# Kernel optimization log

Hardware: AMD Instinct MI355X
Metric: run time of the kernel (lower is better)

Reference implementation:

```python
import jax, jax.numpy as jnp
import numpy as np


def _prelu(x, a):
    return jnp.where(x >= 0, x, a * x)


def _conv1x1(x, w, b, a):
    # x: [N,C,H,W], w: [O,C], b: [O] -> PReLU(conv1x1(x))
    y = jnp.einsum('oc,nchw->nohw', w, x) + b[None, :, None, None]
    return _prelu(y, a)


def setup_inputs() -> dict:
    key = jax.random.key(0)
    ks = jax.random.split(key, 8)
    N, C, H, W = 4, 128, 64, 64
    Cr = C // 2  # reduction=2
    sC = 1.0 / np.sqrt(C)
    x = jax.random.normal(ks[0], (N, C, H, W), dtype=jnp.float32)
    w1 = jax.random.normal(ks[1], (Cr, C), dtype=jnp.float32) * sC
    b1 = jnp.zeros((Cr,), dtype=jnp.float32)
    a1 = jnp.asarray(0.25, dtype=jnp.float32)  # PReLU (single shared slope)
    w2 = jax.random.normal(ks[2], (Cr, C), dtype=jnp.float32) * sC
    b2 = jnp.zeros((Cr,), dtype=jnp.float32)
    a2 = jnp.asarray(0.25, dtype=jnp.float32)
    wa = jax.random.normal(ks[3], (C, C), dtype=jnp.float32) * sC
    ba = jnp.zeros((C,), dtype=jnp.float32)
    aa = jnp.asarray(0.25, dtype=jnp.float32)
    return {"x": x, "w1": w1, "b1": b1, "a1": a1,
            "w2": w2, "b2": b2, "a2": a2,
            "wa": wa, "ba": ba, "aa": aa}


def reference(x, w1, b1, a1, w2, b2, a2, wa, ba, aa):
    N, C, H, W = x.shape
    HW = H * W
    e1 = _conv1x1(x, w1, b1, a1).reshape(N, -1, HW)   # [N,Cr,HW]
    e2 = _conv1x1(x, w2, b2, a2).reshape(N, -1, HW)   # [N,Cr,HW]
    asm = _conv1x1(x, wa, ba, aa).reshape(N, C, HW)   # [N,C,HW]
    # ksize=1: per-channel outer products summed over channels == single contraction
    score = jnp.einsum('nci,ncj->nij', e1, e2)        # [N,HW,HW]
    score = jax.nn.softmax(score, axis=2)
    out = jnp.einsum('nij,ncj->nci', score, asm)      # [N,C,HW]
    return out.reshape(N, C, H, W)
```

## Files before the change

kernel.cpp:

```cpp
#include <hip/hip_runtime.h>
#include <hip/hip_bf16.h>
#include <stdint.h>


typedef float   f32x16 __attribute__((ext_vector_type(16)));
typedef __bf16  bf16x8 __attribute__((ext_vector_type(8)));
typedef __bf16  bf16x2 __attribute__((ext_vector_type(2)));
typedef unsigned int u32x4 __attribute__((ext_vector_type(4)));
typedef unsigned int u32x2 __attribute__((ext_vector_type(2)));

#define L2E 1.4426950408889634f

#define Q_OFF   (0u)
#define KF_OFF  (2u << 20)
#define VF_OFF  (4u << 20)
#define DEN_OFF (8u << 20)
#define WH_OFF  ((8u << 20) + (1u << 19))
#define WL_OFF  (WH_OFF + (1u << 16))
#define OP_OFF  (9u << 20)

__device__ inline unsigned short f2bf(float f) {
  unsigned u = __builtin_bit_cast(unsigned, f);
  return (unsigned short)((u + 0x7FFFu + ((u >> 16) & 1u)) >> 16);
}
__device__ inline float bf2f(unsigned short h) {
  unsigned u = ((unsigned)h) << 16;
  return __builtin_bit_cast(float, u);
}
__device__ inline unsigned pack2(float a, float b) {
  bf16x2 t = { (__bf16)a, (__bf16)b };
  return __builtin_bit_cast(unsigned, t);
}

__device__ inline void gld_lds16(const void* g, void* l) {
  __builtin_amdgcn_global_load_lds(
      (const __attribute__((address_space(1))) unsigned*)g,
      (__attribute__((address_space(3))) unsigned*)l, 16, 0, 0);
}

__global__ void wcast_kernel(const float* __restrict__ w1, const float* __restrict__ w2,
                             const float* __restrict__ wa, char* __restrict__ ws) {
  int idx = blockIdx.x * 256 + threadIdx.x;
  unsigned short* WH = (unsigned short*)(ws + WH_OFF);
  unsigned short* WL = (unsigned short*)(ws + WL_OFF);
#pragma unroll
  for (int r = 0; r < 4; ++r) {
    int i = r * 8192 + idx;
    int oc = i >> 7, c = i & 127;
    float v = oc < 64 ? w1[oc * 128 + c]
            : (oc < 128 ? w2[(oc - 64) * 128 + c] : wa[(oc - 128) * 128 + c]);
    unsigned short h = f2bf(v);
    WH[i] = h;
    WL[i] = f2bf(v - bf2f(h));
  }
}

__global__ __launch_bounds__(256) void conv_kernel(
    const float* __restrict__ x, char* __restrict__ ws,
    const float* __restrict__ b1, const float* __restrict__ a1,
    const float* __restrict__ b2, const float* __restrict__ a2,
    const float* __restrict__ ba, const float* __restrict__ aa) {
  int bid = blockIdx.x;
  int n = bid >> 7, st = bid & 127;
  int sb = st * 32;
  int tid = threadIdx.x;
  int wid = tid >> 6, lane = tid & 63, l31 = lane & 31, hi = lane >> 5;

  __shared__ float xl[128][36];
  __shared__ float tl[2][64][33];
  float* vl = (float*)xl;

  const float* xb = x + (size_t)n * 128 * 4096;
#pragma unroll
  for (int it = 0; it < 4; ++it) {
    int flat4 = tid + 256 * it;
    int c = flat4 >> 3, s4 = flat4 & 7;
    float4 v = *(const float4*)(xb + (size_t)c * 4096 + sb + s4 * 4);
    *(float4*)&xl[c][s4 * 4] = v;
  }
  __syncthreads();

  const char* WH = ws + WH_OFF;
  const char* WL = ws + WL_OFF;
  int oc0 = wid * 64;

  f32x16 acc[2];
  acc[0] = 0.f; acc[1] = 0.f;
#pragma unroll
  for (int c0 = 0; c0 < 8; ++c0) {
    __bf16 eh[8], el[8];
#pragma unroll
    for (int j = 0; j < 8; ++j) {
      float v = xl[c0 * 16 + hi * 8 + j][l31];
      __bf16 h = (__bf16)v;
      eh[j] = h;
      el[j] = (__bf16)(v - (float)h);
    }
    bf16x8 xh = {eh[0], eh[1], eh[2], eh[3], eh[4], eh[5], eh[6], eh[7]};
    bf16x8 xlo = {el[0], el[1], el[2], el[3], el[4], el[5], el[6], el[7]};
#pragma unroll
    for (int mb = 0; mb < 2; ++mb) {
      size_t wo = (size_t)(oc0 + mb * 32 + l31) * 256 + c0 * 32 + hi * 16;
      bf16x8 wh = *(const bf16x8*)(WH + wo);
      bf16x8 wl = *(const bf16x8*)(WL + wo);
      acc[mb] = __builtin_amdgcn_mfma_f32_32x32x16_bf16(wh, xh, acc[mb], 0, 0, 0);
      acc[mb] = __builtin_amdgcn_mfma_f32_32x32x16_bf16(wh, xlo, acc[mb], 0, 0, 0);
      acc[mb] = __builtin_amdgcn_mfma_f32_32x32x16_bf16(wl, xh, acc[mb], 0, 0, 0);
    }
  }
  __syncthreads();

  if (wid < 2) {
    const float* bb = wid ? b2 : b1;
    float slope = wid ? a2[0] : a1[0];
    float scl = wid ? 1.0f : L2E;
#pragma unroll
    for (int mb = 0; mb < 2; ++mb)
#pragma unroll
      for (int reg = 0; reg < 16; ++reg) {
        int row = mb * 32 + (reg & 3) + 8 * (reg >> 2) + 4 * hi;
        float y = acc[mb][reg] + bb[row];
        y = fmaxf(y, 0.f) + slope * fminf(y, 0.f);
        tl[wid][row][l31] = y * scl;
      }
  } else {
    float slope = aa[0];
#pragma unroll
    for (int mb = 0; mb < 2; ++mb)
#pragma unroll
      for (int reg = 0; reg < 16; ++reg) {
        int dv = (wid - 2) * 64 + mb * 32 + (reg & 3) + 8 * (reg >> 2) + 4 * hi;
        float y = acc[mb][reg] + ba[dv];
        y = fmaxf(y, 0.f) + slope * fminf(y, 0.f);
        vl[dv * 33 + l31] = y;
      }
  }
  __syncthreads();

  if (wid == 0) {
    char* Qg = ws + Q_OFF + (size_t)n * (4096 * 128);
#pragma unroll
    for (int it = 0; it < 4; ++it) {
      int sl = (lane >> 3) + it * 8;
      u32x4 pv;
#pragma unroll
      for (int p = 0; p < 4; ++p)
        pv[p] = pack2(tl[0][(lane & 7) * 8 + 2 * p][sl],
                      tl[0][(lane & 7) * 8 + 2 * p + 1][sl]);
      *(u32x4*)(Qg + (size_t)(sb + sl) * 128 + (lane & 7) * 16) = pv;
    }
  } else if (wid == 1) {
    char* KFb = ws + KF_OFF + (size_t)n * (512 << 10);
    int d0 = (lane & 7) >> 1, hs = lane & 1;
#pragma unroll
    for (int it = 0; it < 4; ++it) {
      int sl = (lane >> 3) + it * 8;
      u32x4 pv;
#pragma unroll
      for (int p = 0; p < 4; ++p)
        pv[p] = pack2(tl[1][(lane & 7) * 8 + 2 * p][sl],
                      tl[1][(lane & 7) * 8 + 2 * p + 1][sl]);
      *(u32x4*)(KFb + ((size_t)(st * 4 + d0) * 64 + hs * 32 + sl) * 16) = pv;
    }
  }
  {
    char* VFb = ws + VF_OFF + (size_t)n * (1u << 20);
#pragma unroll
    for (int r = 0; r < 2; ++r) {
      int u = tid + r * 256;
      int dv = u >> 2, sc = u & 3;
      u32x4 pv;
#pragma unroll
      for (int p = 0; p < 4; ++p)
        pv[p] = pack2(vl[dv * 33 + sc * 8 + 2 * p], vl[dv * 33 + sc * 8 + 2 * p + 1]);
      int unit = st * 8 + (dv >> 5) * 2 + (sc >> 1);
      *(u32x4*)(VFb + ((size_t)unit * 64 + (sc & 1) * 32 + (dv & 31)) * 16) = pv;
    }
  }
}

__global__ __launch_bounds__(256, 3) void attn_kernel(char* __restrict__ ws) {
  int bid = blockIdx.x;
  int split = bid & 7;
  int qt = (bid >> 3) & 31;
  int batch = bid >> 8;
  int tid = threadIdx.x;
  int wid = tid >> 6, lane = tid & 63, l31 = lane & 31, hi = lane >> 5;

  const char* Qb  = ws + Q_OFF  + (size_t)batch * (4096 * 128);
  const char* Kt0 = ws + KF_OFF + (size_t)batch * (512 << 10) +
                    (size_t)(split * 16) * 4096;
  const char* Vt0 = ws + VF_OFF + (size_t)batch * (1u << 20) +
                    (size_t)(split * 16) * 8192;

  __shared__ char sbuf[3][12288];

  int q0 = qt * 128 + wid * 32;
  int lo16 = lane * 16;

  bf16x8 qf[4];
#pragma unroll
  for (int d0 = 0; d0 < 4; ++d0)
    qf[d0] = *(const bf16x8*)(Qb + (size_t)(q0 + l31) * 128 + d0 * 32 + hi * 16);

  f32x16 oacc[4];
#pragma unroll
  for (int i = 0; i < 4; ++i) oacc[i] = 0.f;
  float den0 = 0.f, den1 = 0.f;

  auto stage = [&](int b, int t) {
#pragma unroll
    for (int i = 0; i < 3; ++i) {
      int c = wid * 3 + i;
      const char* src = (c < 4) ? Kt0 + (size_t)t * 4096 + c * 1024 + lo16
                                : Vt0 + (size_t)t * 8192 + (c - 4) * 1024 + lo16;
      gld_lds16(src, &sbuf[b][c * 1024]);
    }
  };

  f32x16 sacc[2];
  unsigned pk[8];

  stage(0, 0);
  __syncthreads();
  stage(1, 1);
  {
    f32x16 s;
    s = 0.f;
    __builtin_amdgcn_s_setprio(1);
#pragma unroll
    for (int d0 = 0; d0 < 4; ++d0) {
      bf16x8 kf = *(const bf16x8*)(&sbuf[0][d0 * 1024 + lo16]);
      s = __builtin_amdgcn_mfma_f32_32x32x16_bf16(kf, qf[d0], s, 0, 0, 0);
    }
    __builtin_amdgcn_s_setprio(0);
    sacc[0] = s;
  }
  __syncthreads();
  stage(2, 2);

#pragma unroll
  for (int t = 1; t < 16; ++t) {
    {
      const char* kb = sbuf[t % 3];
      f32x16 s;
      s = 0.f;
      __builtin_amdgcn_s_setprio(1);
#pragma unroll
      for (int d0 = 0; d0 < 4; ++d0) {
        bf16x8 kf = *(const bf16x8*)(kb + d0 * 1024 + lo16);
        s = __builtin_amdgcn_mfma_f32_32x32x16_bf16(kf, qf[d0], s, 0, 0, 0);
      }
      __builtin_amdgcn_s_setprio(0);
      sacc[t & 1] = s;
    }
    {
      f32x16 sp = sacc[(t - 1) & 1];
#pragma unroll
      for (int m = 0; m < 8; ++m) {
        float e0 = __builtin_amdgcn_exp2f(sp[2 * m]);
        float e1 = __builtin_amdgcn_exp2f(sp[2 * m + 1]);
        if (m & 1) den1 += e0 + e1; else den0 += e0 + e1;
        pk[m] = pack2(e0, e1);
      }
    }
    {
      const char* vb = sbuf[(t - 1) % 3] + 4096;
#pragma unroll
      for (int kc = 0; kc < 2; ++kc) {
        const int bs = kc * 4;
        u32x2 r0 = __builtin_amdgcn_permlane32_swap(pk[bs + 0], pk[bs + 2],
                                                    false, false);
        u32x2 r1 = __builtin_amdgcn_permlane32_swap(pk[bs + 1], pk[bs + 3],
                                                    false, false);
        u32x4 pu = {r0.x, r1.x, r0.y, r1.y};
        bf16x8 pf = __builtin_bit_cast(bf16x8, pu);
        __builtin_amdgcn_s_setprio(1);
#pragma unroll
        for (int dvb = 0; dvb < 4; ++dvb) {
          bf16x8 vf = *(const bf16x8*)(vb + (dvb * 2 + kc) * 1024 + lo16);
          oacc[dvb] = __builtin_amdgcn_mfma_f32_32x32x16_bf16(vf, pf,
                                                              oacc[dvb], 0, 0, 0);
        }
        __builtin_amdgcn_s_setprio(0);
      }
    }
    __syncthreads();
    if (t + 2 < 16) stage((t + 2) % 3, t + 2);
  }

  {
    f32x16 sp = sacc[15 & 1];
#pragma unroll
    for (int m = 0; m < 8; ++m) {
      float e0 = __builtin_amdgcn_exp2f(sp[2 * m]);
      float e1 = __builtin_amdgcn_exp2f(sp[2 * m + 1]);
      if (m & 1) den1 += e0 + e1; else den0 += e0 + e1;
      pk[m] = pack2(e0, e1);
    }
    const char* vb = sbuf[15 % 3] + 4096;
#pragma unroll
    for (int kc = 0; kc < 2; ++kc) {
      const int bs = kc * 4;
      u32x2 r0 = __builtin_amdgcn_permlane32_swap(pk[bs + 0], pk[bs + 2],
                                                  false, false);
      u32x2 r1 = __builtin_amdgcn_permlane32_swap(pk[bs + 1], pk[bs + 3],
                                                  false, false);
      u32x4 pu = {r0.x, r1.x, r0.y, r1.y};
      bf16x8 pf = __builtin_bit_cast(bf16x8, pu);
#pragma unroll
      for (int dvb = 0; dvb < 4; ++dvb) {
        bf16x8 vf = *(const bf16x8*)(vb + (dvb * 2 + kc) * 1024 + lo16);
        oacc[dvb] = __builtin_amdgcn_mfma_f32_32x32x16_bf16(vf, pf,
                                                            oacc[dvb], 0, 0, 0);
      }
    }
  }

  unsigned short* OPu = (unsigned short*)(ws + OP_OFF) +
                        (size_t)((batch * 32 + qt) * 8 + split) * 16384;
  int qloc = wid * 32 + l31;
#pragma unroll
  for (int dvb = 0; dvb < 4; ++dvb)
#pragma unroll
    for (int reg = 0; reg < 16; ++reg) {
      int dv = dvb * 32 + (reg & 3) + 8 * (reg >> 2) + 4 * hi;
      OPu[dv * 128 + qloc] = f2bf(oacc[dvb][reg]);
    }
  float den = den0 + den1;
  float dtot = den + __shfl_xor(den, 32, 64);
  if (hi == 0) {
    float* DEN = (float*)(ws + DEN_OFF) +
                 (size_t)((batch * 32 + qt) * 8 + split) * 128;
    DEN[qloc] = dtot;
  }
}

__global__ __launch_bounds__(256) void combine_kernel(const char* __restrict__ ws,
                                                      float* __restrict__ out) {
  int idx8 = (blockIdx.x * 256 + threadIdx.x) * 8;
  int n = idx8 >> 19;
  int dv = (idx8 >> 12) & 127;
  int s0 = idx8 & 4095;
  int qt = s0 >> 7, ql = s0 & 127;
  const unsigned short* OPu = (const unsigned short*)(ws + OP_OFF);
  const float* DEN = (const float*)(ws + DEN_OFF);
  size_t pb = (size_t)((n * 32 + qt) * 8);
  float num[8], den[8];
#pragma unroll
  for (int j = 0; j < 8; ++j) { num[j] = 0.f; den[j] = 0.f; }
#pragma unroll
  for (int h = 0; h < 8; ++h) {
    bf16x8 v = *(const bf16x8*)(OPu + (pb + h) * 16384 + (size_t)dv * 128 + ql);
    const float* dp = DEN + (pb + h) * 128 + ql;
    float4 d0 = *(const float4*)dp;
    float4 d1 = *(const float4*)(dp + 4);
#pragma unroll
    for (int j = 0; j < 8; ++j) num[j] += (float)v[j];
    den[0] += d0.x; den[1] += d0.y; den[2] += d0.z; den[3] += d0.w;
    den[4] += d1.x; den[5] += d1.y; den[6] += d1.z; den[7] += d1.w;
  }
  float4 o0 = {num[0] / den[0], num[1] / den[1], num[2] / den[2], num[3] / den[3]};
  float4 o1 = {num[4] / den[4], num[5] / den[5], num[6] / den[6], num[7] / den[7]};
  *(float4*)&out[idx8] = o0;
  *(float4*)&out[idx8 + 4] = o1;
}

extern "C" void kernel_launch(void* const* d_in, const int* in_sizes, int n_in,
                              void* d_out, int out_size, void* d_ws, size_t ws_size,
                              hipStream_t stream) {
  (void)in_sizes; (void)n_in; (void)out_size; (void)ws_size;
  const float* x  = (const float*)d_in[0];
  const float* w1 = (const float*)d_in[1];
  const float* b1 = (const float*)d_in[2];
  const float* a1 = (const float*)d_in[3];
  const float* w2 = (const float*)d_in[4];
  const float* b2 = (const float*)d_in[5];
  const float* a2 = (const float*)d_in[6];
  const float* wa = (const float*)d_in[7];
  const float* ba = (const float*)d_in[8];
  const float* aa = (const float*)d_in[9];
  char* ws = (char*)d_ws;
  float* out = (float*)d_out;

  wcast_kernel<<<dim3(32), dim3(256), 0, stream>>>(w1, w2, wa, ws);
  conv_kernel<<<dim3(512), dim3(256), 0, stream>>>(x, ws, b1, a1, b2, a2, ba, aa);
  attn_kernel<<<dim3(1024), dim3(256), 0, stream>>>(ws);
  combine_kernel<<<dim3(1024), dim3(256), 0, stream>>>(ws, out);
}
```

Baseline: 66.52 us.

## Double query rows per warp to reuse K/V tiles across two Q subtiles

Each warp now handles 64 query rows (two 32-row subtiles) rather than 32, so each K and V fragment read from LDS feeds two MFMAs. The grid halves to 512 blocks of 256 queries each. The three-stage software pipeline, which overlapped the exp step with the next tile's QK, is replaced by a simpler double-buffered loop. The aim is to halve K/V staging traffic per query, at the cost of more registers (occupancy hint lowered from 3 to 2), fewer blocks, and less overlap between the exp and MFMA work.

```diff
diff --git a/kernel.cpp b/kernel.cpp
--- a/kernel.cpp
+++ b/kernel.cpp
@@ -179,11 +179,11 @@
   }
 }
 
-__global__ __launch_bounds__(256, 3) void attn_kernel(char* __restrict__ ws) {
+__global__ __launch_bounds__(256, 2) void attn_kernel(char* __restrict__ ws) {
   int bid = blockIdx.x;
   int split = bid & 7;
-  int qt = (bid >> 3) & 31;
-  int batch = bid >> 8;
+  int qt = (bid >> 3) & 15;
+  int batch = bid >> 7;
   int tid = threadIdx.x;
   int wid = tid >> 6, lane = tid & 63, l31 = lane & 31, hi = lane >> 5;
 
@@ -193,20 +193,24 @@
   const char* Vt0 = ws + VF_OFF + (size_t)batch * (1u << 20) +
                     (size_t)(split * 16) * 8192;
 
-  __shared__ char sbuf[3][12288];
-
-  int q0 = qt * 128 + wid * 32;
+  __shared__ char sbuf[2][12288];
+
+  int q0 = qt * 256 + wid * 64;
   int lo16 = lane * 16;
 
-  bf16x8 qf[4];
-#pragma unroll
-  for (int d0 = 0; d0 < 4; ++d0)
-    qf[d0] = *(const bf16x8*)(Qb + (size_t)(q0 + l31) * 128 + d0 * 32 + hi * 16);
-
-  f32x16 oacc[4];
-#pragma unroll
-  for (int i = 0; i < 4; ++i) oacc[i] = 0.f;
-  float den0 = 0.f, den1 = 0.f;
+  bf16x8 qf0[4], qf1[4];
+#pragma unroll
+  for (int d0 = 0; d0 < 4; ++d0) {
+    qf0[d0] = *(const bf16x8*)(Qb + (size_t)(q0 + l31) * 128 + d0 * 32 + hi * 16);
+    qf1[d0] = *(const bf16x8*)(Qb + (size_t)(q0 + 32 + l31) * 128 + d0 * 32 + hi * 16);
+  }
+
+  f32x16 oacc[2][4];
+#pragma unroll
+  for (int qs = 0; qs < 2; ++qs)
+#pragma unroll
+    for (int i = 0; i < 4; ++i) oacc[qs][i] = 0.f;
+  float denA = 0.f, denB = 0.f;
 
   auto stage = [&](int b, int t) {
 #pragma unroll
@@ -218,121 +222,87 @@
     }
   };
 
-  f32x16 sacc[2];
-  unsigned pk[8];
-
   stage(0, 0);
   __syncthreads();
-  stage(1, 1);
-  {
-    f32x16 s;
-    s = 0.f;
+
+  for (int t = 0; t < 16; ++t) {
+    if (t + 1 < 16) stage((t + 1) & 1, t + 1);
+    const char* kb = sbuf[t & 1];
+    const char* vb = kb + 4096;
+
+    f32x16 s0, s1;
+    s0 = 0.f; s1 = 0.f;
     __builtin_amdgcn_s_setprio(1);
 #pragma unroll
     for (int d0 = 0; d0 < 4; ++d0) {
-      bf16x8 kf = *(const bf16x8*)(&sbuf[0][d0 * 1024 + lo16]);
-      s = __builtin_amdgcn_mfma_f32_32x32x16_bf16(kf, qf[d0], s, 0, 0, 0);
+      bf16x8 kf = *(const bf16x8*)(kb + d0 * 1024 + lo16);
+      s0 = __builtin_amdgcn_mfma_f32_32x32x16_bf16(kf, qf0[d0], s0, 0, 0, 0);
+      s1 = __builtin_amdgcn_mfma_f32_32x32x16_bf16(kf, qf1[d0], s1, 0, 0, 0);
     }
     __builtin_amdgcn_s_setprio(0);
-    sacc[0] = s;
-  }
-  __syncthreads();
-  stage(2, 2);
-
-#pragma unroll
-  for (int t = 1; t < 16; ++t) {
-    {
-      const char* kb = sbuf[t % 3];
-      f32x16 s;
-      s = 0.f;
+
+    unsigned pk0[8], pk1[8];
+#pragma unroll
+    for (int m = 0; m < 8; ++m) {
+      float a0 = __builtin_amdgcn_exp2f(s0[2 * m]);
+      float a1 = __builtin_amdgcn_exp2f(s0[2 * m + 1]);
+      denA += a0 + a1;
+      pk0[m] = pack2(a0, a1);
+      float b0 = __builtin_amdgcn_exp2f(s1[2 * m]);
+      float b1 = __builtin_amdgcn_exp2f(s1[2 * m + 1]);
+      denB += b0 + b1;
+      pk1[m] = pack2(b0, b1);
+    }
+
+#pragma unroll
+    for (int kc = 0; kc < 2; ++kc) {
+      const int bs = kc * 4;
+      u32x2 r0 = __builtin_amdgcn_permlane32_swap(pk0[bs + 0], pk0[bs + 2],
+                                                  false, false);
+      u32x2 r1 = __builtin_amdgcn_permlane32_swap(pk0[bs + 1], pk0[bs + 3],
+                                                  false, false);
+      u32x4 pu0 = {r0.x, r1.x, r0.y, r1.y};
+      bf16x8 pf0 = __builtin_bit_cast(bf16x8, pu0);
+      u32x2 r2 = __builtin_amdgcn_permlane32_swap(pk1[bs + 0], pk1[bs + 2],
+                                                  false, false);
+      u32x2 r3 = __builtin_amdgcn_permlane32_swap(pk1[bs + 1], pk1[bs + 3],
+                                                  false, false);
+      u32x4 pu1 = {r2.x, r3.x, r2.y, r3.y};
+      bf16x8 pf1 = __builtin_bit_cast(bf16x8, pu1);
       __builtin_amdgcn_s_setprio(1);
 #pragma unroll
-      for (int d0 = 0; d0 < 4; ++d0) {
-        bf16x8 kf = *(const bf16x8*)(kb + d0 * 1024 + lo16);
-        s = __builtin_amdgcn_mfma_f32_32x32x16_bf16(kf, qf[d0], s, 0, 0, 0);
+      for (int dvb = 0; dvb < 4; ++dvb) {
+        bf16x8 vf = *(const bf16x8*)(vb + (dvb * 2 + kc) * 1024 + lo16);
+        oacc[0][dvb] = __builtin_amdgcn_mfma_f32_32x32x16_bf16(vf, pf0,
+                                                               oacc[0][dvb], 0, 0, 0);
+        oacc[1][dvb] = __builtin_amdgcn_mfma_f32_32x32x16_bf16(vf, pf1,
+                                                               oacc[1][dvb], 0, 0, 0);
       }
       __builtin_amdgcn_s_setprio(0);
-      sacc[t & 1] = s;
-    }
-    {
-      f32x16 sp = sacc[(t - 1) & 1];
-#pragma unroll
-      for (int m = 0; m < 8; ++m) {
-        float e0 = __builtin_amdgcn_exp2f(sp[2 * m]);
-        float e1 = __builtin_amdgcn_exp2f(sp[2 * m + 1]);
-        if (m & 1) den1 += e0 + e1; else den0 += e0 + e1;
-        pk[m] = pack2(e0, e1);
+    }
+
+    __syncthreads();
+  }
+
+  unsigned short* OPu = (unsigned short*)(ws + OP_OFF) +
+                        (size_t)((batch * 16 + qt) * 8 + split) * 32768;
+#pragma unroll
+  for (int qs = 0; qs < 2; ++qs) {
+    int qloc = wid * 64 + qs * 32 + l31;
+#pragma unroll
+    for (int dvb = 0; dvb < 4; ++dvb)
+#pragma unroll
+      for (int reg = 0; reg < 16; ++reg) {
+        int dv = dvb * 32 + (reg & 3) + 8 * (reg >> 2) + 4 * hi;
+        OPu[dv * 256 + qloc] = f2bf(oacc[qs][dvb][reg]);
       }
-    }
-    {
-      const char* vb = sbuf[(t - 1) % 3] + 4096;
-#pragma unroll
-      for (int kc = 0; kc < 2; ++kc) {
-        const int bs = kc * 4;
-        u32x2 r0 = __builtin_amdgcn_permlane32_swap(pk[bs + 0], pk[bs + 2],
-                                                    false, false);
-        u32x2 r1 = __builtin_amdgcn_permlane32_swap(pk[bs + 1], pk[bs + 3],
-                                                    false, false);
-        u32x4 pu = {r0.x, r1.x, r0.y, r1.y};
-        bf16x8 pf = __builtin_bit_cast(bf16x8, pu);
-        __builtin_amdgcn_s_setprio(1);
-#pragma unroll
-        for (int dvb = 0; dvb < 4; ++dvb) {
-          bf16x8 vf = *(const bf16x8*)(vb + (dvb * 2 + kc) * 1024 + lo16);
-          oacc[dvb] = __builtin_amdgcn_mfma_f32_32x32x16_bf16(vf, pf,
-                                                              oacc[dvb], 0, 0, 0);
-        }
-        __builtin_amdgcn_s_setprio(0);
-      }
-    }
-    __syncthreads();
-    if (t + 2 < 16) stage((t + 2) % 3, t + 2);
-  }
-
-  {
-    f32x16 sp = sacc[15 & 1];
-#pragma unroll
-    for (int m = 0; m < 8; ++m) {
-      float e0 = __builtin_amdgcn_exp2f(sp[2 * m]);
-      float e1 = __builtin_amdgcn_exp2f(sp[2 * m + 1]);
-      if (m & 1) den1 += e0 + e1; else den0 += e0 + e1;
-      pk[m] = pack2(e0, e1);
-    }
-    const char* vb = sbuf[15 % 3] + 4096;
-#pragma unroll
-    for (int kc = 0; kc < 2; ++kc) {
-      const int bs = kc * 4;
-      u32x2 r0 = __builtin_amdgcn_permlane32_swap(pk[bs + 0], pk[bs + 2],
-                                                  false, false);
-      u32x2 r1 = __builtin_amdgcn_permlane32_swap(pk[bs + 1], pk[bs + 3],
-                                                  false, false);
-      u32x4 pu = {r0.x, r1.x, r0.y, r1.y};
-      bf16x8 pf = __builtin_bit_cast(bf16x8, pu);
-#pragma unroll
-      for (int dvb = 0; dvb < 4; ++dvb) {
-        bf16x8 vf = *(const bf16x8*)(vb + (dvb * 2 + kc) * 1024 + lo16);
-        oacc[dvb] = __builtin_amdgcn_mfma_f32_32x32x16_bf16(vf, pf,
-                                                            oacc[dvb], 0, 0, 0);
-      }
-    }
-  }
-
-  unsigned short* OPu = (unsigned short*)(ws + OP_OFF) +
-                        (size_t)((batch * 32 + qt) * 8 + split) * 16384;
-  int qloc = wid * 32 + l31;
-#pragma unroll
-  for (int dvb = 0; dvb < 4; ++dvb)
-#pragma unroll
-    for (int reg = 0; reg < 16; ++reg) {
-      int dv = dvb * 32 + (reg & 3) + 8 * (reg >> 2) + 4 * hi;
-      OPu[dv * 128 + qloc] = f2bf(oacc[dvb][reg]);
-    }
-  float den = den0 + den1;
-  float dtot = den + __shfl_xor(den, 32, 64);
-  if (hi == 0) {
-    float* DEN = (float*)(ws + DEN_OFF) +
-                 (size_t)((batch * 32 + qt) * 8 + split) * 128;
-    DEN[qloc] = dtot;
+    float den = qs ? denB : denA;
+    float dtot = den + __shfl_xor(den, 32, 64);
+    if (hi == 0) {
+      float* DEN = (float*)(ws + DEN_OFF) +
+                   (size_t)((batch * 16 + qt) * 8 + split) * 256;
+      DEN[qloc] = dtot;
+    }
   }
 }
 
@@ -342,17 +312,17 @@
   int n = idx8 >> 19;
   int dv = (idx8 >> 12) & 127;
   int s0 = idx8 & 4095;
-  int qt = s0 >> 7, ql = s0 & 127;
+  int qt = s0 >> 8, ql = s0 & 255;
   const unsigned short* OPu = (const unsigned short*)(ws + OP_OFF);
   const float* DEN = (const float*)(ws + DEN_OFF);
-  size_t pb = (size_t)((n * 32 + qt) * 8);
+  size_t pb = (size_t)((n * 16 + qt) * 8);
   float num[8], den[8];
 #pragma unroll
   for (int j = 0; j < 8; ++j) { num[j] = 0.f; den[j] = 0.f; }
 #pragma unroll
   for (int h = 0; h < 8; ++h) {
-    bf16x8 v = *(const bf16x8*)(OPu + (pb + h) * 16384 + (size_t)dv * 128 + ql);
-    const float* dp = DEN + (pb + h) * 128 + ql;
+    bf16x8 v = *(const bf16x8*)(OPu + (pb + h) * 32768 + (size_t)dv * 256 + ql);
+    const float* dp = DEN + (pb + h) * 256 + ql;
     float4 d0 = *(const float4*)dp;
     float4 d1 = *(const float4*)(dp + 4);
 #pragma unroll
@@ -385,6 +355,6 @@
 
   wcast_kernel<<<dim3(32), dim3(256), 0, stream>>>(w1, w2, wa, ws);
   conv_kernel<<<dim3(512), dim3(256), 0, stream>>>(x, ws, b1, a1, b2, a2, ba, aa);
-  attn_kernel<<<dim3(1024), dim3(256), 0, stream>>>(ws);
+  attn_kernel<<<dim3(512), dim3(256), 0, stream>>>(ws);
   combine_kernel<<<dim3(1024), dim3(256), 0, stream>>>(ws, out);
 }
```

New measurement: 63.66 us. -4.3%, faster.
